# Performance work log

Hardware: AMD Instinct MI355X
Metric: run time of the kernel (lower is better)

## Reference

```python
import jax, jax.numpy as jnp
import numpy as np

DIM = 384
NUM_HEADS = 6
HEAD_DIM = DIM // NUM_HEADS
MLP_HIDDEN = 4 * DIM
SCALE = HEAD_DIM ** -0.5
EPS = 1e-5


def layer_norm(x, w, b):
    mu = jnp.mean(x, axis=-1, keepdims=True)
    var = jnp.mean(jnp.square(x - mu), axis=-1, keepdims=True)
    return (x - mu) * jax.lax.rsqrt(var + EPS) * w + b


def setup_inputs() -> dict:
    key = jax.random.key(0)
    ks = jax.random.split(key, 24)
    d = DIM
    s = 0.02
    inp = {
        'x1': jax.random.normal(ks[0], (16, d, 32, 32), jnp.float32),
        'x2': jax.random.normal(ks[1], (16, d, 32, 32), jnp.float32),
        # per-branch attention-input LayerNorm + kqv projection (no bias)
        'ln_a1_w': jnp.ones((d,), jnp.float32), 'ln_a1_b': jnp.zeros((d,), jnp.float32),
        'kqv1_w': jax.random.normal(ks[2], (d, 3 * d), jnp.float32) * s,
        'ln_a2_w': jnp.ones((d,), jnp.float32), 'ln_a2_b': jnp.zeros((d,), jnp.float32),
        'kqv2_w': jax.random.normal(ks[3], (d, 3 * d), jnp.float32) * s,
        # output projections
        'proj1_w': jax.random.normal(ks[4], (d, d), jnp.float32) * s,
        'proj1_b': jnp.zeros((d,), jnp.float32),
        'proj2_w': jax.random.normal(ks[5], (d, d), jnp.float32) * s,
        'proj2_b': jnp.zeros((d,), jnp.float32),
        # post-attention LayerNorms
        'ln1_w': jnp.ones((d,), jnp.float32), 'ln1_b': jnp.zeros((d,), jnp.float32),
        'ln2_w': jnp.ones((d,), jnp.float32), 'ln2_b': jnp.zeros((d,), jnp.float32),
        # MLPs
        'mlp1_fc1_w': jax.random.normal(ks[6], (d, MLP_HIDDEN), jnp.float32) * s,
        'mlp1_fc1_b': jnp.zeros((MLP_HIDDEN,), jnp.float32),
        'mlp1_fc2_w': jax.random.normal(ks[7], (MLP_HIDDEN, d), jnp.float32) * s,
        'mlp1_fc2_b': jnp.zeros((d,), jnp.float32),
        'mlp2_fc1_w': jax.random.normal(ks[8], (d, MLP_HIDDEN), jnp.float32) * s,
        'mlp2_fc1_b': jnp.zeros((MLP_HIDDEN,), jnp.float32),
        'mlp2_fc2_w': jax.random.normal(ks[9], (MLP_HIDDEN, d), jnp.float32) * s,
        'mlp2_fc2_b': jnp.zeros((d,), jnp.float32),
    }
    return inp


def _kqv_branch(x, ln_w, ln_b, Wkqv):
    # x: [B, C, H, W] -> embedding [B, N, C]; k,q,v: [B, h, N, hd]
    B, C, H, W = x.shape
    N = H * W
    emb = x.reshape(B, C, N).transpose(0, 2, 1)
    xn = layer_norm(emb, ln_w, ln_b)
    kqv = (xn @ Wkqv).reshape(B, N, 3, NUM_HEADS, HEAD_DIM).transpose(2, 0, 3, 1, 4)
    return kqv[0], kqv[1], kqv[2], emb


def _cross_attn(q, k, v):
    # q,k,v: [B, h, N, hd] -> [B, N, C]
    scores = jnp.einsum('bhnd,bhmd->bhnm', q, k) * SCALE
    a = jax.nn.softmax(scores, axis=-1)
    o = jnp.einsum('bhnm,bhmd->bhnd', a, v)
    B, h, N, hd = o.shape
    return o.transpose(0, 2, 1, 3).reshape(B, N, h * hd)


def reference(x1, x2, ln_a1_w, ln_a1_b, kqv1_w, ln_a2_w, ln_a2_b, kqv2_w,
              proj1_w, proj1_b, proj2_w, proj2_b, ln1_w, ln1_b, ln2_w, ln2_b,
              mlp1_fc1_w, mlp1_fc1_b, mlp1_fc2_w, mlp1_fc2_b,
              mlp2_fc1_w, mlp2_fc1_b, mlp2_fc2_w, mlp2_fc2_b):
    B, C, H, W = x1.shape
    k1, q1, v1, emb1 = _kqv_branch(x1, ln_a1_w, ln_a1_b, kqv1_w)
    k2, q2, v2, emb2 = _kqv_branch(x2, ln_a2_w, ln_a2_b, kqv2_w)
    a1 = _cross_attn(q1, k2, v2)   # branch 1 queries attend to branch 2
    a2 = _cross_attn(q2, k1, v1)
    out1 = emb1 + (a1 @ proj1_w + proj1_b)
    h1 = layer_norm(out1, ln1_w, ln1_b)
    out1 = out1 + (jax.nn.gelu(h1 @ mlp1_fc1_w + mlp1_fc1_b, approximate=False) @ mlp1_fc2_w + mlp1_fc2_b)
    out2 = emb2 + (a2 @ proj2_w + proj2_b)
    h2 = layer_norm(out2, ln2_w, ln2_b)
    out2 = out2 + (jax.nn.gelu(h2 @ mlp2_fc1_w + mlp2_fc1_b, approximate=False) @ mlp2_fc2_w + mlp2_fc2_b)
    out1 = out1.transpose(0, 2, 1).reshape(B, C, H, W)
    out2 = out2.transpose(0, 2, 1).reshape(B, C, H, W)
    return (out1, out2)
```

## Files before the change

### kernel.cpp

```cpp
#include <hip/hip_runtime.h>
#include <math.h>

typedef unsigned short u16;
typedef __attribute__((ext_vector_type(8))) short short8;
typedef __attribute__((ext_vector_type(4))) short short4b;
typedef __attribute__((ext_vector_type(4))) float f32x4;

#define MFMA(a,b,c) __builtin_amdgcn_mfma_f32_16x16x32_bf16(a, b, c, 0, 0, 0)
#define SWZ(row, ch) ((((ch) ^ ((row) & 7)) << 3))
#define EXP2F(x) __builtin_amdgcn_exp2f(x)

#define BARRIER() do {                                          \
    asm volatile("s_waitcnt lgkmcnt(0)" ::: "memory");          \
    __builtin_amdgcn_s_barrier();                               \
    __builtin_amdgcn_sched_barrier(0);                          \
} while (0)

static __device__ __forceinline__ f32x4 MFMA16(short4b a, short4b b, f32x4 c) {
#if __has_builtin(__builtin_amdgcn_mfma_f32_16x16x16bf16_1k)
    return __builtin_amdgcn_mfma_f32_16x16x16bf16_1k(a, b, c, 0, 0, 0);
#else
    f32x4 d;
    asm volatile("v_mfma_f32_16x16x16_bf16 %0, %1, %2, %3\n\ts_nop 7"
                 : "=v"(d) : "v"(a), "v"(b), "v"(c));
    return d;
#endif
}

__device__ __forceinline__ float b2f(u16 v) {
    union { unsigned int i; float f; } c; c.i = ((unsigned int)v) << 16; return c.f;
}
__device__ __forceinline__ u16 f2b(float f) {
    union { float f; unsigned int i; } c; c.f = f;
    unsigned int u = c.i;
    return (u16)((u + 0x7fffu + ((u >> 16) & 1u)) >> 16);
}
__device__ __forceinline__ u16 f2b_p(float f) {
    union { float f; unsigned int i; } c; c.f = f;
    return (u16)((c.i + 0x8000u) >> 16);
}

struct TWArgs { const float* src[8]; u16* dst[8]; int K[8]; int N[8]; };

__global__ __launch_bounds__(256) void transpose_w(TWArgs a) {
    int wi = blockIdx.z;
    int K = a.K[wi], N = a.N[wi];
    int n0 = blockIdx.x * 32, k0 = blockIdx.y * 32;
    if (n0 >= N || k0 >= K) return;
    __shared__ float t[32][33];
    const float* s = a.src[wi]; u16* d = a.dst[wi];
    int tx = threadIdx.x & 31, ty = threadIdx.x >> 5;
    for (int i = 0; i < 32; i += 8)
        t[ty + i][tx] = s[(size_t)(k0 + ty + i) * N + n0 + tx];
    __syncthreads();
    for (int i = 0; i < 32; i += 8)
        d[(size_t)(n0 + ty + i) * K + k0 + tx] = f2b(t[tx][ty + i]);
}

__global__ __launch_bounds__(256)
void ln_tr(const float* __restrict__ x0, const float* __restrict__ x1,
           const float* __restrict__ w0, const float* __restrict__ bb0,
           const float* __restrict__ w1, const float* __restrict__ bb1,
           u16* __restrict__ xn0, u16* __restrict__ xn1) {
    int br = blockIdx.z;
    const float* x  = br ? x1 : x0;
    const float* wv = br ? w1 : w0;
    const float* bv = br ? bb1 : bb0;
    u16* xn = br ? xn1 : xn0;
    int b = blockIdx.y, n0 = blockIdx.x * 32;
    __shared__ float tile[32][385];
    __shared__ float smu[32], srs[32];
    int tid = threadIdx.x;
    const float* xb = x + (size_t)b * 384 * 1024 + n0;
    for (int idx = tid; idx < 384 * 32; idx += 256) {
        int c = idx >> 5, nn = idx & 31;
        tile[nn][c] = xb[(size_t)c * 1024 + nn];
    }
    __syncthreads();
    {
        int nn = tid >> 3, part = tid & 7;
        float s1 = 0.f, s2 = 0.f;
        for (int c = part * 48; c < part * 48 + 48; ++c) {
            float v = tile[nn][c]; s1 += v; s2 += v * v;
        }
        for (int off = 1; off < 8; off <<= 1) {
            s1 += __shfl_xor(s1, off, 64); s2 += __shfl_xor(s2, off, 64);
        }
        if (part == 0) {
            float mu = s1 * (1.f / 384.f);
            float var = s2 * (1.f / 384.f) - mu * mu;
            smu[nn] = mu; srs[nn] = rsqrtf(fmaxf(var, 0.f) + 1e-5f);
        }
    }
    __syncthreads();
    size_t rowbase = (size_t)b * 1024 + n0;
    for (int idx = tid; idx < 32 * 384; idx += 256) {
        int nn = idx / 384, c = idx - nn * 384;
        float v = tile[nn][c];
        float g = (v - smu[nn]) * srs[nn] * wv[c] + bv[c];
        xn[(rowbase + nn) * 384 + c] = f2b(g);
    }
}

__global__ __launch_bounds__(256)
void ln_rows(const float* __restrict__ i0, const float* __restrict__ i1,
             const float* __restrict__ w0, const float* __restrict__ bb0,
             const float* __restrict__ w1, const float* __restrict__ bb1,
             u16* __restrict__ o0, u16* __restrict__ o1) {
    int br = blockIdx.z;
    const float* in = br ? i1 : i0;
    const float* wv = br ? w1 : w0;
    const float* bv = br ? bb1 : bb0;
    u16* out = br ? o1 : o0;
    int w = threadIdx.x >> 6, l = threadIdx.x & 63;
    size_t row = (size_t)blockIdx.x * 4 + w;
    const float* p = in + row * 384;
    float v[6]; float s1 = 0.f, s2 = 0.f;
    #pragma unroll
    for (int j = 0; j < 6; j++) { v[j] = p[j * 64 + l]; s1 += v[j]; s2 += v[j] * v[j]; }
    for (int off = 1; off < 64; off <<= 1) {
        s1 += __shfl_xor(s1, off, 64); s2 += __shfl_xor(s2, off, 64);
    }
    float mu = s1 * (1.f / 384.f);
    float var = s2 * (1.f / 384.f) - mu * mu;
    float rs = rsqrtf(fmaxf(var, 0.f) + 1e-5f);
    #pragma unroll
    for (int j = 0; j < 6; j++) {
        int c = j * 64 + l;
        out[row * 384 + c] = f2b((v[j] - mu) * rs * wv[c] + bv[c]);
    }
}

template <int EPI>
__global__ __launch_bounds__(256)
void gemm128(const u16* __restrict__ A0, const u16* __restrict__ A1,
             const u16* __restrict__ B0, const u16* __restrict__ B1,
             void* C0v, void* C1v,
             const float* __restrict__ bias0, const float* __restrict__ bias1,
             const void* R0v, const void* R1v,
             int N, int K) {
    const int br = blockIdx.z;
    const u16* A = br ? A1 : A0;
    const u16* B = br ? B1 : B0;
    void* Cv = br ? C1v : C0v;
    const float* bias = br ? bias1 : bias0;
    const void* Rv = br ? R1v : R0v;

    const int n0 = blockIdx.x * 128;
    const int m0 = blockIdx.y * 128;
    const int tid = threadIdx.x;
    const int w = tid >> 6, l = tid & 63;
    const int wm = w >> 1, wn = w & 1;
    const int lr = l & 15, lq = l >> 4;

    __shared__ alignas(16) u16 As[2][128 * 40];
    __shared__ alignas(16) u16 Bs[2][128 * 40];

    f32x4 acc[4][4];
    #pragma unroll
    for (int i = 0; i < 4; i++)
        #pragma unroll
        for (int j = 0; j < 4; j++) acc[i][j] = (f32x4)0.0f;

    const int ar0 = tid >> 2, ac0 = (tid & 3) * 8;
    const int ar1 = ar0 + 64;
    const u16* Ap0 = A + (size_t)(m0 + ar0) * K + ac0;
    const u16* Ap1 = A + (size_t)(m0 + ar1) * K + ac0;
    const u16* Bp0 = B + (size_t)(n0 + ar0) * K + ac0;
    const u16* Bp1 = B + (size_t)(n0 + ar1) * K + ac0;

    const int nk = K >> 5;
    uint4 pa0 = *(const uint4*)Ap0, pa1 = *(const uint4*)Ap1;
    uint4 pb0 = *(const uint4*)Bp0, pb1 = *(const uint4*)Bp1;
    *(uint4*)&As[0][ar0 * 40 + ac0] = pa0;
    *(uint4*)&As[0][ar1 * 40 + ac0] = pa1;
    *(uint4*)&Bs[0][ar0 * 40 + ac0] = pb0;
    *(uint4*)&Bs[0][ar1 * 40 + ac0] = pb1;
    pa0 = *(const uint4*)(Ap0 + 32); pa1 = *(const uint4*)(Ap1 + 32);
    pb0 = *(const uint4*)(Bp0 + 32); pb1 = *(const uint4*)(Bp1 + 32);
    __syncthreads();

    for (int kt = 0; kt < nk; ++kt) {
        const int cur = kt & 1;
        if (kt + 1 < nk) {
            const int nx = cur ^ 1;
            *(uint4*)&As[nx][ar0 * 40 + ac0] = pa0;
            *(uint4*)&As[nx][ar1 * 40 + ac0] = pa1;
            *(uint4*)&Bs[nx][ar0 * 40 + ac0] = pb0;
            *(uint4*)&Bs[nx][ar1 * 40 + ac0] = pb1;
        }
        if (kt + 2 < nk) {
            const int kb = (kt + 2) * 32;
            pa0 = *(const uint4*)(Ap0 + kb); pa1 = *(const uint4*)(Ap1 + kb);
            pb0 = *(const uint4*)(Bp0 + kb); pb1 = *(const uint4*)(Bp1 + kb);
        }
        short8 af[4], bf[4];
        #pragma unroll
        for (int mt = 0; mt < 4; ++mt)
            af[mt] = *(const short8*)&As[cur][(wm * 64 + mt * 16 + lr) * 40 + lq * 8];
        #pragma unroll
        for (int nt = 0; nt < 4; ++nt)
            bf[nt] = *(const short8*)&Bs[cur][(wn * 64 + nt * 16 + lr) * 40 + lq * 8];
        #pragma unroll
        for (int mt = 0; mt < 4; ++mt)
            #pragma unroll
            for (int nt = 0; nt < 4; ++nt)
                acc[mt][nt] = MFMA(af[mt], bf[nt], acc[mt][nt]);
        __syncthreads();
    }

    #pragma unroll
    for (int mt = 0; mt < 4; ++mt)
        #pragma unroll
        for (int nt = 0; nt < 4; ++nt) {
            const int col = n0 + wn * 64 + nt * 16 + lr;
            const int rbase = m0 + wm * 64 + mt * 16 + lq * 4;
            const float bv = (EPI == 0) ? 0.f : bias[col];
            #pragma unroll
            for (int r = 0; r < 4; r++) {
                const int row = rbase + r;
                const size_t idx = (size_t)row * N + col;
                float v = acc[mt][nt][r];
                if (EPI == 0) {
                    if (col < 768) {
                        ((u16*)Cv)[idx] = f2b(col >= 384 ? v * 0.18033688f : v);
                    } else {
                        u16* vtb = (u16*)Rv;
                        vtb[((((size_t)(row >> 10)) * 6 + ((col - 768) >> 6)) * 64
                             + (col & 63)) * 1024 + (row & 1023)] = f2b(v);
                    }
                } else if (EPI == 1) {
                    float xr = ((const float*)Rv)[
                        ((size_t)(row >> 10) * 384 + col) * 1024 + (row & 1023)];
                    ((float*)Cv)[idx] = v + bv + xr;
                } else if (EPI == 2) {
                    v += bv;
                    float g = 0.5f * v * (1.f + erff(v * 0.70710678118f));
                    ((u16*)Cv)[idx] = f2b(g);
                } else {
                    ((float*)Cv)[idx] = v + bv + ((const float*)Rv)[idx];
                }
            }
        }
}

__global__ __launch_bounds__(256)
void attn_k(const u16* __restrict__ kqvA, const u16* __restrict__ kqvB,
            const u16* __restrict__ vtA, const u16* __restrict__ vtB,
            u16* __restrict__ oA, u16* __restrict__ oB) {
    const int bid = blockIdx.x;
    const int g = bid & 7, qb = (bid >> 3) & 7, s = bid >> 6;
    const int grp = s * 8 + g;
    const int ob = grp & 1, h = (grp >> 1) % 6, b = grp / 12;

    const u16* kqvQ  = (ob ? kqvB : kqvA) + (size_t)b * 1024 * 1152;
    const u16* kqvKV = (ob ? kqvA : kqvB) + (size_t)b * 1024 * 1152;
    const u16* vt    = (ob ? vtA : vtB) + ((size_t)b * 6 + h) * 64 * 1024;
    u16* outp = (ob ? oB : oA) + (size_t)b * 1024 * 384;
    const u16* qp = kqvQ + 384 + h * 64;
    const u16* kp = kqvKV + h * 64;

    __shared__ alignas(16) u16 Ks[2][64 * 64];
    __shared__ alignas(16) u16 Vts[2][64 * 64];

    const int tid = threadIdx.x, w = tid >> 6, l = tid & 63;
    const int lr = l & 15, lq = l >> 4;

    short8 qf[2][2];
    #pragma unroll
    for (int a = 0; a < 2; a++)
        #pragma unroll
        for (int ks = 0; ks < 2; ks++)
            qf[a][ks] = *(const short8*)&qp[
                (size_t)(qb * 128 + w * 32 + a * 16 + lr) * 1152 + ks * 32 + lq * 8];

    const int srow = tid >> 3, sch = tid & 7;
    uint4 kpre[2][2], vpre[2][2];
    #pragma unroll
    for (int t = 0; t < 2; t++)
        #pragma unroll
        for (int i = 0; i < 2; i++) {
            int row = srow + i * 32;
            kpre[t][i] = *(const uint4*)&kp[(size_t)(t * 64 + row) * 1152 + sch * 8];
            vpre[t][i] = *(const uint4*)&vt[(size_t)row * 1024 + t * 64 + sch * 8];
        }

    #pragma unroll
    for (int i = 0; i < 2; i++) {
        int row = srow + i * 32;
        int o = row * 64 + SWZ(row, sch);
        *(uint4*)&Ks[0][o] = kpre[0][i];
        *(uint4*)&Vts[0][o] = vpre[0][i];
    }
    #pragma unroll
    for (int i = 0; i < 2; i++) {
        int row = srow + i * 32;
        kpre[0][i] = *(const uint4*)&kp[(size_t)(2 * 64 + row) * 1152 + sch * 8];
        vpre[0][i] = *(const uint4*)&vt[(size_t)row * 1024 + 2 * 64 + sch * 8];
    }

    f32x4 oacc[2][4];
    float psum[2] = {0.f, 0.f};
    #pragma unroll
    for (int a = 0; a < 2; a++)
        #pragma unroll
        for (int n = 0; n < 4; n++) oacc[a][n] = (f32x4)0.0f;

    BARRIER();

    for (int jt = 0; jt < 16; ++jt) {
        const int cur = jt & 1, nx = cur ^ 1;
        if (jt + 1 < 16) {
            #pragma unroll
            for (int i = 0; i < 2; i++) {
                int row = srow + i * 32;
                int o = row * 64 + SWZ(row, sch);
                *(uint4*)&Ks[nx][o] = kpre[nx][i];
                *(uint4*)&Vts[nx][o] = vpre[nx][i];
            }
            if (jt + 3 < 16) {
                #pragma unroll
                for (int i = 0; i < 2; i++) {
                    int row = srow + i * 32;
                    kpre[nx][i] = *(const uint4*)&kp[(size_t)((jt + 3) * 64 + row) * 1152 + sch * 8];
                    vpre[nx][i] = *(const uint4*)&vt[(size_t)row * 1024 + (jt + 3) * 64 + sch * 8];
                }
            }
        }

        f32x4 sacc[4][2];
        #pragma unroll
        for (int kb = 0; kb < 4; kb++)
            #pragma unroll
            for (int a = 0; a < 2; a++) sacc[kb][a] = (f32x4)0.0f;
        __builtin_amdgcn_s_setprio(1);
        #pragma unroll
        for (int ks = 0; ks < 2; ++ks) {
            short8 bk[4];
            #pragma unroll
            for (int kb = 0; kb < 4; kb++) {
                int row = kb * 16 + lr;
                bk[kb] = *(const short8*)&Ks[cur][row * 64 + SWZ(row, ks * 4 + lq)];
            }
            #pragma unroll
            for (int kb = 0; kb < 4; kb++)
                #pragma unroll
                for (int a = 0; a < 2; a++)
                    sacc[kb][a] = MFMA(bk[kb], qf[a][ks], sacc[kb][a]);
        }
        __builtin_amdgcn_s_setprio(0);

        short4b ap16[2][4];
        #pragma unroll
        for (int a = 0; a < 2; a++)
            #pragma unroll
            for (int kb = 0; kb < 4; kb++) {
                f32x4 s4 = sacc[kb][a];
                float p0 = EXP2F(s4[0]), p1 = EXP2F(s4[1]);
                float p2 = EXP2F(s4[2]), p3 = EXP2F(s4[3]);
                psum[a] += (p0 + p1) + (p2 + p3);
                short4b pk;
                pk[0] = (short)f2b_p(p0); pk[1] = (short)f2b_p(p1);
                pk[2] = (short)f2b_p(p2); pk[3] = (short)f2b_p(p3);
                ap16[a][kb] = pk;
            }

        __builtin_amdgcn_s_setprio(1);
        #pragma unroll
        for (int kb = 0; kb < 4; ++kb) {
            short4b bv16[4];
            #pragma unroll
            for (int n = 0; n < 4; n++) {
                int row = n * 16 + lr;
                int addr = row * 64 + SWZ(row, kb * 2 + (lq >> 1)) + (lq & 1) * 4;
                bv16[n] = *(const short4b*)&Vts[cur][addr];
            }
            #pragma unroll
            for (int a = 0; a < 2; a++)
                #pragma unroll
                for (int n = 0; n < 4; n++)
                    oacc[a][n] = MFMA16(ap16[a][kb], bv16[n], oacc[a][n]);
        }
        __builtin_amdgcn_s_setprio(0);
        BARRIER();
    }

    #pragma unroll
    for (int a = 0; a < 2; a++) {
        psum[a] += __shfl_xor(psum[a], 16, 64);
        psum[a] += __shfl_xor(psum[a], 32, 64);
        psum[a] = 1.f / psum[a];
    }
    float rec[2][4];
    #pragma unroll
    for (int a = 0; a < 2; a++)
        #pragma unroll
        for (int r = 0; r < 4; r++)
            rec[a][r] = __shfl(psum[a], lq * 4 + r, 64);

    u16* Ot = &Ks[0][0];
    #pragma unroll
    for (int a = 0; a < 2; a++)
        #pragma unroll
        for (int n = 0; n < 4; n++)
            #pragma unroll
            for (int r = 0; r < 4; r++) {
                int row = w * 32 + a * 16 + lq * 4 + r;
                int col = n * 16 + lr;
                Ot[row * 64 + SWZ(row, col >> 3) + (col & 7)] =
                    f2b(oacc[a][n][r] * rec[a][r]);
            }
    BARRIER();
    #pragma unroll
    for (int it = 0; it < 4; it++) {
        int id = it * 256 + tid;
        int row = id >> 3, c16 = id & 7;
        uint4 v = *(const uint4*)&Ot[row * 64 + SWZ(row, c16)];
        *(uint4*)&outp[(size_t)(qb * 128 + row) * 384 + h * 64 + c16 * 8] = v;
    }
}

__global__ __launch_bounds__(256)
void transpose_out(const float* __restrict__ r0, const float* __restrict__ r1,
                   float* __restrict__ out) {
    int z = blockIdx.z, ob = z >> 4, b = z & 15;
    const float* rp = ob ? r1 : r0;
    int c0 = blockIdx.y * 32, n0 = blockIdx.x * 32;
    __shared__ float t[32][33];
    int tx = threadIdx.x & 31, ty = threadIdx.x >> 5;
    for (int i = 0; i < 32; i += 8)
        t[ty + i][tx] = rp[((size_t)b * 1024 + n0 + ty + i) * 384 + c0 + tx];
    __syncthreads();
    for (int i = 0; i < 32; i += 8)
        out[(size_t)ob * 6291456 + ((size_t)b * 384 + c0 + ty + i) * 1024 + n0 + tx]
            = t[tx][ty + i];
}

extern "C" void kernel_launch(void* const* d_in, const int* in_sizes, int n_in,
                              void* d_out, int out_size, void* d_ws, size_t ws_size,
                              hipStream_t stream) {
    const float* x1      = (const float*)d_in[0];
    const float* x2      = (const float*)d_in[1];
    const float* ln_a1_w = (const float*)d_in[2];
    const float* ln_a1_b = (const float*)d_in[3];
    const float* kqv1_w  = (const float*)d_in[4];
    const float* ln_a2_w = (const float*)d_in[5];
    const float* ln_a2_b = (const float*)d_in[6];
    const float* kqv2_w  = (const float*)d_in[7];
    const float* proj1_w = (const float*)d_in[8];
    const float* proj1_b = (const float*)d_in[9];
    const float* proj2_w = (const float*)d_in[10];
    const float* proj2_b = (const float*)d_in[11];
    const float* ln1_w   = (const float*)d_in[12];
    const float* ln1_b   = (const float*)d_in[13];
    const float* ln2_w   = (const float*)d_in[14];
    const float* ln2_b   = (const float*)d_in[15];
    const float* m1f1w   = (const float*)d_in[16];
    const float* m1f1b   = (const float*)d_in[17];
    const float* m1f2w   = (const float*)d_in[18];
    const float* m1f2b   = (const float*)d_in[19];
    const float* m2f1w   = (const float*)d_in[20];
    const float* m2f1b   = (const float*)d_in[21];
    const float* m2f2w   = (const float*)d_in[22];
    const float* m2f2b   = (const float*)d_in[23];
    (void)in_sizes; (void)n_in; (void)out_size; (void)ws_size;

    const size_t R = 16384;
    char* ws = (char*)d_ws;
    size_t off = 0;
    auto alloc = [&](size_t bytes) -> char* {
        char* p = ws + off;
        off = (off + bytes + 255) & ~(size_t)255;
        return p;
    };
    u16* kqv1t  = (u16*)alloc(1152 * 384 * 2);
    u16* kqv2t  = (u16*)alloc(1152 * 384 * 2);
    u16* proj1t = (u16*)alloc(384 * 384 * 2);
    u16* proj2t = (u16*)alloc(384 * 384 * 2);
    u16* fc11t  = (u16*)alloc(1536 * 384 * 2);
    u16* fc12t  = (u16*)alloc(1536 * 384 * 2);
    u16* fc21t  = (u16*)alloc(384 * 1536 * 2);
    u16* fc22t  = (u16*)alloc(384 * 1536 * 2);
    u16* xn1 = (u16*)alloc(R * 384 * 2);
    u16* xn2 = (u16*)alloc(R * 384 * 2);
    char* regC = alloc(R * 1152 * 2 * 2);
    u16* kqv1 = (u16*)regC;
    u16* kqv2 = (u16*)(regC + R * 1152 * 2);
    float* oa1 = (float*)regC;
    float* oa2 = (float*)(regC + R * 384 * 4);
    u16* hid_b2 = (u16*)(regC + 2 * R * 384 * 4);
    u16* at1 = (u16*)d_out;
    u16* at2 = at1 + R * 384;
    u16* vt1 = at2 + R * 384;
    u16* vt2 = vt1 + (size_t)16 * 6 * 64 * 1024;
    u16* hid_b1 = (u16*)d_out;

    TWArgs tw;
    tw.src[0] = kqv1_w;  tw.dst[0] = kqv1t;  tw.K[0] = 384;  tw.N[0] = 1152;
    tw.src[1] = kqv2_w;  tw.dst[1] = kqv2t;  tw.K[1] = 384;  tw.N[1] = 1152;
    tw.src[2] = proj1_w; tw.dst[2] = proj1t; tw.K[2] = 384;  tw.N[2] = 384;
    tw.src[3] = proj2_w; tw.dst[3] = proj2t; tw.K[3] = 384;  tw.N[3] = 384;
    tw.src[4] = m1f1w;   tw.dst[4] = fc11t;  tw.K[4] = 384;  tw.N[4] = 1536;
    tw.src[5] = m2f1w;   tw.dst[5] = fc12t;  tw.K[5] = 384;  tw.N[5] = 1536;
    tw.src[6] = m1f2w;   tw.dst[6] = fc21t;  tw.K[6] = 1536; tw.N[6] = 384;
    tw.src[7] = m2f2w;   tw.dst[7] = fc22t;  tw.K[7] = 1536; tw.N[7] = 384;
    transpose_w<<<dim3(48, 48, 8), dim3(256), 0, stream>>>(tw);

    ln_tr<<<dim3(32, 16, 2), dim3(256), 0, stream>>>(
        x1, x2, ln_a1_w, ln_a1_b, ln_a2_w, ln_a2_b, xn1, xn2);

    gemm128<0><<<dim3(9, 128, 2), dim3(256), 0, stream>>>(
        xn1, xn2, kqv1t, kqv2t, (void*)kqv1, (void*)kqv2,
        (const float*)nullptr, (const float*)nullptr,
        (const void*)vt1, (const void*)vt2, 1152, 384);

    attn_k<<<dim3(1536), dim3(256), 0, stream>>>(kqv1, kqv2, vt1, vt2, at1, at2);

    gemm128<1><<<dim3(3, 128, 2), dim3(256), 0, stream>>>(
        at1, at2, proj1t, proj2t, (void*)oa1, (void*)oa2,
        proj1_b, proj2_b, (const void*)x1, (const void*)x2, 384, 384);

    ln_rows<<<dim3(4096, 1, 2), dim3(256), 0, stream>>>(
        oa1, oa2, ln1_w, ln1_b, ln2_w, ln2_b, xn1, xn2);

    for (int half = 0; half < 2; ++half) {
        const size_t ro = (size_t)half * 8192;
        gemm128<2><<<dim3(12, 64, 2), dim3(256), 0, stream>>>(
            xn1 + ro * 384, xn2 + ro * 384, fc11t, fc12t,
            (void*)hid_b1, (void*)hid_b2, m1f1b, m2f1b, nullptr, nullptr, 1536, 384);
        gemm128<3><<<dim3(3, 64, 2), dim3(256), 0, stream>>>(
            hid_b1, hid_b2, fc21t, fc22t,
            (void*)(oa1 + ro * 384), (void*)(oa2 + ro * 384),
            m1f2b, m2f2b, (const void*)(oa1 + ro * 384), (const void*)(oa2 + ro * 384),
            384, 1536);
    }

    transpose_out<<<dim3(32, 12, 32), dim3(256), 0, stream>>>(oa1, oa2, (float*)d_out);
}
```

Measured before the change: 627.5 us.

## Software-pipeline attention QK^T one tile ahead and vectorize LayerNorm transpose IO

```diff
diff --git a/kernel.cpp b/kernel.cpp
--- a/kernel.cpp
+++ b/kernel.cpp
@@ -72,9 +72,11 @@
     __shared__ float smu[32], srs[32];
     int tid = threadIdx.x;
     const float* xb = x + (size_t)b * 384 * 1024 + n0;
-    for (int idx = tid; idx < 384 * 32; idx += 256) {
-        int c = idx >> 5, nn = idx & 31;
-        tile[nn][c] = xb[(size_t)c * 1024 + nn];
+    for (int idx = tid; idx < 384 * 8; idx += 256) {
+        int c = idx >> 3, q = idx & 7;
+        const float4 v = *(const float4*)&xb[(size_t)c * 1024 + q * 4];
+        tile[q * 4 + 0][c] = v.x; tile[q * 4 + 1][c] = v.y;
+        tile[q * 4 + 2][c] = v.z; tile[q * 4 + 3][c] = v.w;
     }
     __syncthreads();
     {
@@ -94,11 +96,16 @@
     }
     __syncthreads();
     size_t rowbase = (size_t)b * 1024 + n0;
-    for (int idx = tid; idx < 32 * 384; idx += 256) {
-        int nn = idx / 384, c = idx - nn * 384;
-        float v = tile[nn][c];
-        float g = (v - smu[nn]) * srs[nn] * wv[c] + bv[c];
-        xn[(rowbase + nn) * 384 + c] = f2b(g);
+    for (int idx = tid; idx < 1536; idx += 256) {
+        int nn = idx / 48, c0 = (idx - nn * 48) * 8;
+        float mu = smu[nn], rs = srs[nn];
+        u16 ov[8];
+        #pragma unroll
+        for (int k = 0; k < 8; k++) {
+            int c = c0 + k;
+            ov[k] = f2b((tile[nn][c] - mu) * rs * wv[c] + bv[c]);
+        }
+        *(uint4*)&xn[(rowbase + nn) * 384 + c0] = *(uint4*)ov;
     }
 }
 
@@ -244,6 +251,71 @@
         }
 }
 
+__device__ __forceinline__ void qkt_frag(f32x4 (&sacc)[4][2], const u16* Ksb,
+                                         const short8 (&qf)[2][2],
+                                         int lr, int lq) {
+    #pragma unroll
+    for (int kb = 0; kb < 4; kb++)
+        #pragma unroll
+        for (int a = 0; a < 2; a++) sacc[kb][a] = (f32x4)0.0f;
+    __builtin_amdgcn_s_setprio(1);
+    #pragma unroll
+    for (int ks = 0; ks < 2; ++ks) {
+        short8 bk[4];
+        #pragma unroll
+        for (int kb = 0; kb < 4; kb++) {
+            int row = kb * 16 + lr;
+            bk[kb] = *(const short8*)&Ksb[row * 64 + SWZ(row, ks * 4 + lq)];
+        }
+        #pragma unroll
+        for (int kb = 0; kb < 4; kb++)
+            #pragma unroll
+            for (int a = 0; a < 2; a++)
+                sacc[kb][a] = MFMA(bk[kb], qf[a][ks], sacc[kb][a]);
+    }
+    __builtin_amdgcn_s_setprio(0);
+}
+
+__device__ __forceinline__ void sm_frag(short4b (&ap16)[2][4],
+                                        const f32x4 (&sacc)[4][2],
+                                        float (&psum)[2]) {
+    #pragma unroll
+    for (int a = 0; a < 2; a++)
+        #pragma unroll
+        for (int kb = 0; kb < 4; kb++) {
+            f32x4 s4 = sacc[kb][a];
+            float p0 = EXP2F(s4[0]), p1 = EXP2F(s4[1]);
+            float p2 = EXP2F(s4[2]), p3 = EXP2F(s4[3]);
+            psum[a] += (p0 + p1) + (p2 + p3);
+            short4b pk;
+            pk[0] = (short)f2b_p(p0); pk[1] = (short)f2b_p(p1);
+            pk[2] = (short)f2b_p(p2); pk[3] = (short)f2b_p(p3);
+            ap16[a][kb] = pk;
+        }
+}
+
+__device__ __forceinline__ void pv_frag(f32x4 (&oacc)[2][4],
+                                        const short4b (&ap16)[2][4],
+                                        const u16* Vtsb, int lr, int lq) {
+    __builtin_amdgcn_s_setprio(1);
+    #pragma unroll
+    for (int kb = 0; kb < 4; ++kb) {
+        short4b bv16[4];
+        #pragma unroll
+        for (int n = 0; n < 4; n++) {
+            int row = n * 16 + lr;
+            int addr = row * 64 + SWZ(row, kb * 2 + (lq >> 1)) + (lq & 1) * 4;
+            bv16[n] = *(const short4b*)&Vtsb[addr];
+        }
+        #pragma unroll
+        for (int a = 0; a < 2; a++)
+            #pragma unroll
+            for (int n = 0; n < 4; n++)
+                oacc[a][n] = MFMA16(ap16[a][kb], bv16[n], oacc[a][n]);
+    }
+    __builtin_amdgcn_s_setprio(0);
+}
+
 __global__ __launch_bounds__(256)
 void attn_k(const u16* __restrict__ kqvA, const u16* __restrict__ kqvB,
             const u16* __restrict__ vtA, const u16* __restrict__ vtB,
@@ -276,27 +348,25 @@
 
     const int srow = tid >> 3, sch = tid & 7;
     uint4 kpre[2][2], vpre[2][2];
-    #pragma unroll
-    for (int t = 0; t < 2; t++)
-        #pragma unroll
-        for (int i = 0; i < 2; i++) {
-            int row = srow + i * 32;
-            kpre[t][i] = *(const uint4*)&kp[(size_t)(t * 64 + row) * 1152 + sch * 8];
-            vpre[t][i] = *(const uint4*)&vt[(size_t)row * 1024 + t * 64 + sch * 8];
-        }
 
     #pragma unroll
     for (int i = 0; i < 2; i++) {
         int row = srow + i * 32;
+        uint4 k0 = *(const uint4*)&kp[(size_t)row * 1152 + sch * 8];
+        uint4 k1 = *(const uint4*)&kp[(size_t)(64 + row) * 1152 + sch * 8];
+        uint4 v0 = *(const uint4*)&vt[(size_t)row * 1024 + sch * 8];
         int o = row * 64 + SWZ(row, sch);
-        *(uint4*)&Ks[0][o] = kpre[0][i];
-        *(uint4*)&Vts[0][o] = vpre[0][i];
+        *(uint4*)&Ks[0][o] = k0;
+        *(uint4*)&Ks[1][o] = k1;
+        *(uint4*)&Vts[0][o] = v0;
     }
     #pragma unroll
     for (int i = 0; i < 2; i++) {
         int row = srow + i * 32;
-        kpre[0][i] = *(const uint4*)&kp[(size_t)(2 * 64 + row) * 1152 + sch * 8];
-        vpre[0][i] = *(const uint4*)&vt[(size_t)row * 1024 + 2 * 64 + sch * 8];
+        kpre[0][i] = *(const uint4*)&kp[(size_t)(128 + row) * 1152 + sch * 8];
+        kpre[1][i] = *(const uint4*)&kp[(size_t)(192 + row) * 1152 + sch * 8];
+        vpre[1][i] = *(const uint4*)&vt[(size_t)row * 1024 + 64 + sch * 8];
+        vpre[0][i] = *(const uint4*)&vt[(size_t)row * 1024 + 128 + sch * 8];
     }
 
     f32x4 oacc[2][4];
@@ -308,81 +378,82 @@
 
     BARRIER();
 
-    for (int jt = 0; jt < 16; ++jt) {
-        const int cur = jt & 1, nx = cur ^ 1;
-        if (jt + 1 < 16) {
-            #pragma unroll
-            for (int i = 0; i < 2; i++) {
-                int row = srow + i * 32;
-                int o = row * 64 + SWZ(row, sch);
-                *(uint4*)&Ks[nx][o] = kpre[nx][i];
-                *(uint4*)&Vts[nx][o] = vpre[nx][i];
-            }
-            if (jt + 3 < 16) {
-                #pragma unroll
-                for (int i = 0; i < 2; i++) {
-                    int row = srow + i * 32;
-                    kpre[nx][i] = *(const uint4*)&kp[(size_t)((jt + 3) * 64 + row) * 1152 + sch * 8];
-                    vpre[nx][i] = *(const uint4*)&vt[(size_t)row * 1024 + (jt + 3) * 64 + sch * 8];
-                }
-            }
-        }
-
-        f32x4 sacc[4][2];
-        #pragma unroll
-        for (int kb = 0; kb < 4; kb++)
-            #pragma unroll
-            for (int a = 0; a < 2; a++) sacc[kb][a] = (f32x4)0.0f;
-        __builtin_amdgcn_s_setprio(1);
-        #pragma unroll
-        for (int ks = 0; ks < 2; ++ks) {
-            short8 bk[4];
-            #pragma unroll
-            for (int kb = 0; kb < 4; kb++) {
-                int row = kb * 16 + lr;
-                bk[kb] = *(const short8*)&Ks[cur][row * 64 + SWZ(row, ks * 4 + lq)];
-            }
-            #pragma unroll
-            for (int kb = 0; kb < 4; kb++)
-                #pragma unroll
-                for (int a = 0; a < 2; a++)
-                    sacc[kb][a] = MFMA(bk[kb], qf[a][ks], sacc[kb][a]);
-        }
-        __builtin_amdgcn_s_setprio(0);
-
-        short4b ap16[2][4];
-        #pragma unroll
-        for (int a = 0; a < 2; a++)
-            #pragma unroll
-            for (int kb = 0; kb < 4; kb++) {
-                f32x4 s4 = sacc[kb][a];
-                float p0 = EXP2F(s4[0]), p1 = EXP2F(s4[1]);
-                float p2 = EXP2F(s4[2]), p3 = EXP2F(s4[3]);
-                psum[a] += (p0 + p1) + (p2 + p3);
-                short4b pk;
-                pk[0] = (short)f2b_p(p0); pk[1] = (short)f2b_p(p1);
-                pk[2] = (short)f2b_p(p2); pk[3] = (short)f2b_p(p3);
-                ap16[a][kb] = pk;
-            }
-
-        __builtin_amdgcn_s_setprio(1);
-        #pragma unroll
-        for (int kb = 0; kb < 4; ++kb) {
-            short4b bv16[4];
-            #pragma unroll
-            for (int n = 0; n < 4; n++) {
-                int row = n * 16 + lr;
-                int addr = row * 64 + SWZ(row, kb * 2 + (lq >> 1)) + (lq & 1) * 4;
-                bv16[n] = *(const short4b*)&Vts[cur][addr];
-            }
-            #pragma unroll
-            for (int a = 0; a < 2; a++)
-                #pragma unroll
-                for (int n = 0; n < 4; n++)
-                    oacc[a][n] = MFMA16(ap16[a][kb], bv16[n], oacc[a][n]);
-        }
-        __builtin_amdgcn_s_setprio(0);
-        BARRIER();
+    f32x4 saccA[4][2], saccB[4][2];
+    qkt_frag(saccA, &Ks[0][0], qf, lr, lq);
+    BARRIER();
+
+    short4b ap16[2][4];
+    for (int jj = 0; jj < 16; jj += 2) {
+        {
+            const int j = jj;
+            if (j + 1 < 16) qkt_frag(saccB, &Ks[1][0], qf, lr, lq);
+            if (j + 2 < 16) {
+                #pragma unroll
+                for (int i = 0; i < 2; i++) {
+                    int row = srow + i * 32;
+                    *(uint4*)&Ks[0][row * 64 + SWZ(row, sch)] = kpre[0][i];
+                }
+            }
+            if (j + 1 < 16) {
+                #pragma unroll
+                for (int i = 0; i < 2; i++) {
+                    int row = srow + i * 32;
+                    *(uint4*)&Vts[1][row * 64 + SWZ(row, sch)] = vpre[1][i];
+                }
+            }
+            if (j + 4 < 16) {
+                #pragma unroll
+                for (int i = 0; i < 2; i++) {
+                    int row = srow + i * 32;
+                    kpre[0][i] = *(const uint4*)&kp[(size_t)((j + 4) * 64 + row) * 1152 + sch * 8];
+                }
+            }
+            if (j + 3 < 16) {
+                #pragma unroll
+                for (int i = 0; i < 2; i++) {
+                    int row = srow + i * 32;
+                    vpre[1][i] = *(const uint4*)&vt[(size_t)row * 1024 + (j + 3) * 64 + sch * 8];
+                }
+            }
+            sm_frag(ap16, saccA, psum);
+            pv_frag(oacc, ap16, &Vts[0][0], lr, lq);
+            BARRIER();
+        }
+        {
+            const int j = jj + 1;
+            if (j + 1 < 16) qkt_frag(saccA, &Ks[0][0], qf, lr, lq);
+            if (j + 2 < 16) {
+                #pragma unroll
+                for (int i = 0; i < 2; i++) {
+                    int row = srow + i * 32;
+                    *(uint4*)&Ks[1][row * 64 + SWZ(row, sch)] = kpre[1][i];
+                }
+            }
+            if (j + 1 < 16) {
+                #pragma unroll
+                for (int i = 0; i < 2; i++) {
+                    int row = srow + i * 32;
+                    *(uint4*)&Vts[0][row * 64 + SWZ(row, sch)] = vpre[0][i];
+                }
+            }
+            if (j + 4 < 16) {
+                #pragma unroll
+                for (int i = 0; i < 2; i++) {
+                    int row = srow + i * 32;
+                    kpre[1][i] = *(const uint4*)&kp[(size_t)((j + 4) * 64 + row) * 1152 + sch * 8];
+                }
+            }
+            if (j + 3 < 16) {
+                #pragma unroll
+                for (int i = 0; i < 2; i++) {
+                    int row = srow + i * 32;
+                    vpre[0][i] = *(const uint4*)&vt[(size_t)row * 1024 + (j + 3) * 64 + sch * 8];
+                }
+            }
+            sm_frag(ap16, saccB, psum);
+            pv_frag(oacc, ap16, &Vts[1][0], lr, lq);
+            BARRIER();
+        }
     }
 
     #pragma unroll
```

New measurement: 633.1 us. No clear change (+0.9%).
